# Kernel tuning notes

Hardware: AMD Instinct MI355X
Metric: run time of the kernel (lower is better)

Reference implementation:

```python
import jax, jax.numpy as jnp
import numpy as np


def _safe_norm(d):
    # Euclidean norm over last axis with torch-style subgradient 0 at 0
    sq = jnp.sum(d * d, axis=-1)
    pos = sq > 0
    return jnp.where(pos, jnp.sqrt(jnp.where(pos, sq, 1.0)), 0.0)


def setup_inputs() -> dict:
    key = jax.random.key(0)
    k1, k2 = jax.random.split(key)
    B, n = 8, 256
    src = jax.random.uniform(k1, (B, n, 2), dtype=jnp.float32) * 2.0 - 1.0
    dst = jax.random.uniform(k2, (B, n, 2), dtype=jnp.float32) * 2.0 - 1.0
    return {"src": src, "dst": dst, "s": 256}


def reference(src, dst, s):
    B, n, _ = src.shape
    dt = src.dtype
    # evaluation grid, matching torch.meshgrid(indexing='ij') then stack((ix,iy))
    lin = jnp.linspace(-1.0, 1.0, s, dtype=dt)
    iy, ix = jnp.meshgrid(lin, lin, indexing="ij")
    gs = jnp.stack((ix, iy), axis=2).reshape(1, -1, 2)  # (1, s*s, 2)

    # TPS system: L wv = rhs
    delta = src[:, :, None, :] - src[:, None, :, :]          # (B,n,n,2)
    K = _safe_norm(delta)                                     # (B,n,n)
    P = jnp.concatenate([jnp.ones((B, n, 1), dt), src], 2)    # (B,n,3)
    top = jnp.concatenate([K, P], 2)                          # (B,n,n+3)
    bot = jnp.concatenate([jnp.swapaxes(P, 1, 2),
                           jnp.zeros((B, 3, 3), dt)], 2)      # (B,3,n+3)
    L = jnp.concatenate([top, bot], 1)                        # (B,n+3,n+3)
    rhs = jnp.concatenate([dst, jnp.zeros((B, 3, 2), dt)], 1) # (B,n+3,2)
    wv = jnp.linalg.solve(L, rhs)                             # (B,n+3,2)

    # evaluate warp on the grid
    S = s * s
    dg = gs[:, :, None, :] - src[:, None, :, :]               # (B,S,n,2)
    Kg = _safe_norm(dg)                                       # (B,S,n)
    gsb = jnp.broadcast_to(gs, (B, S, 2))
    Pg = jnp.concatenate([jnp.ones((B, S, 1), dt), gsb], 2)   # (B,S,3)
    Lg = jnp.concatenate([Kg, Pg], 2)                         # (B,S,n+3)
    out = jnp.matmul(Lg, wv)                                  # (B,S,2)
    return out.reshape(B, s, s, 2).transpose(0, 3, 1, 2)
```

## Files before the change

kernel.cpp:

```cpp
#include <hip/hip_runtime.h>
#include <math.h>

#define NCTRL 256
#define NA    259
#define NAUG  261
#define APITCH 264
#define BATCH 8
#define SGRID 256
#define NB    32
#define NPAN  9
#define PPITCH 36
#define PY    4

template<int NBC, int NW>
__device__ __forceinline__ void flat_engine(
    float (&rr)[NBC], const int rows, const int nb, const int width,
    const int tid, const int lane, const int wid,
    float (*panout)[PPITCH], float (*ftmp)[PPITCH], int* permout,
    float (*redrow)[NW][PPITCH], float (*redv)[NW], int (*redi)[NW],
    int* scanw)
{
  bool chosen = false;
  int chosenstep = 0;
  for (int j = 0; j < nb; ++j){
    const int par = j & 1;
    const bool active = (tid < rows) && !chosen;
    float bv = active ? fabsf(rr[0]) : -1.0f;
    int bi = tid;
    #pragma unroll
    for (int off = 32; off; off >>= 1){
      float ov = __shfl_xor(bv, off);
      int   oi = __shfl_xor(bi, off);
      if (ov > bv || (ov == bv && oi < bi)){ bv = ov; bi = oi; }
    }
    if (tid == bi){
      redv[par][wid] = bv; redi[par][wid] = bi;
      #pragma unroll
      for (int q = 0; q < NBC/4; ++q){
        float4 v; v.x=rr[4*q]; v.y=rr[4*q+1]; v.z=rr[4*q+2]; v.w=rr[4*q+3];
        *(float4*)&redrow[par][wid][4*q] = v;
      }
    }
    __syncthreads();
    float gv = redv[par][0]; int gw = 0;
    #pragma unroll
    for (int w = 1; w < NW; ++w){
      if (redv[par][w] > gv ||
          (redv[par][w] == gv && redi[par][w] < redi[par][gw])){
        gv = redv[par][w]; gw = w;
      }
    }
    const int gbi = redi[par][gw];
    float pr[NBC];
    #pragma unroll
    for (int q = 0; q < NBC/4; ++q){
      float4 v = *(const float4*)&redrow[par][gw][4*q];
      pr[4*q]=v.x; pr[4*q+1]=v.y; pr[4*q+2]=v.z; pr[4*q+3]=v.w;
    }
    if (tid < width - j) panout[j][j + tid] = redrow[par][gw][tid];
    if (tid == gbi){ chosen = true; chosenstep = j; }
    if (active && tid != gbi){
      const float rpiv = 1.0f / pr[0];
      const float f = rr[0] * rpiv;
      ftmp[tid][j] = f;
      #pragma unroll
      for (int c = 0; c < NBC-1; ++c)
        rr[c] = fmaf(-f, pr[c+1], rr[c+1]);
    }
  }
  {
    int x = (tid < rows && !chosen) ? 1 : 0;
    int sPS = x;
    #pragma unroll
    for (int off = 1; off < 64; off <<= 1){
      int o = __shfl_up(sPS, off);
      if (lane >= off) sPS += o;
    }
    if (lane == 63) scanw[wid] = sPS;
    __syncthreads();
    int base = 0;
    for (int w = 0; w < wid; ++w) base += scanw[w];
    if (tid < rows){
      const int newloc = chosen ? chosenstep : (nb + base + sPS - x);
      permout[newloc] = tid;
      const int lim = chosen ? chosenstep : nb;
      for (int c = 0; c < lim; ++c) panout[newloc][c] = ftmp[tid][c];
    }
  }
  __syncthreads();
}

__global__ __launch_bounds__(320) void build_panel0(const float* __restrict__ src,
                                                    const float* __restrict__ dst,
                                                    float* __restrict__ A,
                                                    int* __restrict__ permbuf){
  const int b = blockIdx.x;
  float* Ab = A + (size_t)b*NA*APITCH;
  const int tid  = threadIdx.x;
  const int lane = tid & 63;
  const int wid  = tid >> 6;

  __shared__ float pan[NA][PPITCH];
  __shared__ float ftmp[NA][PPITCH];
  __shared__ int   perm[NA];
  __shared__ float redrow[2][5][PPITCH];
  __shared__ float redv[2][5];
  __shared__ int   redi[2][5], scanw[5];
  __shared__ float sx[NCTRL], sy[NCTRL];

  if (tid < NCTRL){
    float2 v = ((const float2*)(src + b*NCTRL*2))[tid];
    sx[tid] = v.x; sy[tid] = v.y;
  }
  __syncthreads();
  {
    const float* db = dst + b*NCTRL*2;
    for (int idx = tid; idx < NA*APITCH; idx += 320){
      int r = idx / APITCH;
      int c = idx - r*APITCH;
      float v = 0.0f;
      if (r < NCTRL){
        if (c < NCTRL){
          float dx = sx[r] - sx[c];
          float dy = sy[r] - sy[c];
          v = __builtin_amdgcn_sqrtf(fmaf(dx, dx, dy*dy));
        } else if (c == NCTRL)   v = 1.0f;
        else if (c == NCTRL+1)   v = sx[r];
        else if (c == NCTRL+2)   v = sy[r];
        else if (c == NA)        v = db[2*r];
        else if (c == NA+1)      v = db[2*r+1];
      } else if (c < NCTRL){
        v = (r == NCTRL) ? 1.0f : ((r == NCTRL+1) ? sx[c] : sy[c]);
      }
      Ab[idx] = v;
      if (c < NB) pan[r][c] = v;
    }
  }
  __syncthreads();

  float rr[NB];
  if (tid < NA){
    #pragma unroll
    for (int q = 0; q < 8; ++q){
      float4 v = *(const float4*)&pan[tid][4*q];
      rr[4*q]=v.x; rr[4*q+1]=v.y; rr[4*q+2]=v.z; rr[4*q+3]=v.w;
    }
  } else {
    #pragma unroll
    for (int c = 0; c < NB; ++c) rr[c] = 0.0f;
  }
  __syncthreads();

  flat_engine<NB,5>(rr, NA, NB, NB, tid, lane, wid,
                    pan, ftmp, perm, redrow, redv, redi, scanw);

  for (int i = tid; i < NA; i += 320) permbuf[b*(NPAN*NA) + i] = perm[i];
  for (int idx = tid; idx < NA*8; idx += 320){
    int i = idx >> 3, q = idx & 7;
    *(float4*)(Ab + (size_t)i*APITCH + 4*q) = *(const float4*)&pan[i][4*q];
  }
}

template<bool LOOK, int NBCN>
__global__ __launch_bounds__(256) void update_kernel(float* __restrict__ A,
                                                     int* __restrict__ permbuf,
                                                     int k0, int pidx, int sb,
                                                     int nbn, int wdn, int wbw){
  const int rows = NA - k0;
  const int ctop = k0 + NB;
  const int tc   = NAUG - ctop;
  const int b    = blockIdx.x / sb;
  const int s    = blockIdx.x - b*sb;
  const int c0   = s*32;
  const int W    = (tc - c0 < 32) ? (tc - c0) : 32;
  float* Ab = A + (size_t)b*NA*APITCH;
  const int tid  = threadIdx.x;
  const int lane = tid & 63;
  const int wid  = tid >> 6;

  __shared__ float pan[NA][PPITCH];
  __shared__ float stage[NA][PPITCH];
  __shared__ float ustg[NB][PPITCH];
  __shared__ int   perm[NA];
  __shared__ float redrow[2][4][PPITCH];
  __shared__ float redv[2][4];
  __shared__ int   redi[2][4], scanw[4];

  for (int i = tid; i < rows; i += 256)
    perm[i] = permbuf[b*(NPAN*NA) + pidx*NA + i];
  for (int idx = tid; idx < rows*8; idx += 256){
    int i = idx >> 3, q = idx & 7;
    *(float4*)&pan[i][4*q] =
      *(const float4*)(Ab + (size_t)(k0+i)*APITCH + k0 + 4*q);
  }
  __syncthreads();

  for (int idx = tid; idx < rows*W; idx += 256){
    int i = idx / W, c = idx - i*W;
    stage[i][c] = Ab[(size_t)(k0+perm[i])*APITCH + ctop + c0 + c];
  }
  __syncthreads();

  if (tid < W){
    float u[NB];
    #pragma unroll
    for (int m = 0; m < NB; ++m) u[m] = stage[m][tid];
    #pragma unroll
    for (int m = 0; m < NB; ++m){
      #pragma unroll
      for (int jj = m+1; jj < NB; ++jj)
        u[jj] = fmaf(-pan[jj][m], u[m], u[jj]);
    }
    #pragma unroll
    for (int m = 0; m < NB; ++m){
      ustg[m][tid] = u[m];
      Ab[(size_t)(k0+m)*APITCH + ctop + c0 + tid] = u[m];
    }
  }
  __syncthreads();

  const int R = rows - NB;
  if (R > 0){
    const int rt = (R + 3) >> 2, ct = (W + 3) >> 2;
    for (int t = tid; t < rt*ct; t += 256){
      int tr = t / ct, tcc = t - tr*ct;
      int i0 = tr*4, cc0 = tcc*4;
      const bool full = (cc0 + 4 <= W);
      int ir[4];
      #pragma unroll
      for (int r = 0; r < 4; ++r){
        int i = i0 + r;
        ir[r] = (i < R) ? i : (R - 1);
      }
      float acc[4][4];
      #pragma unroll
      for (int r = 0; r < 4; ++r){
        if (full){
          float4 v = *(const float4*)&stage[NB + ir[r]][cc0];
          acc[r][0]=v.x; acc[r][1]=v.y; acc[r][2]=v.z; acc[r][3]=v.w;
        } else {
          #pragma unroll
          for (int c = 0; c < 4; ++c)
            acc[r][c] = (cc0 + c < W) ? stage[NB + ir[r]][cc0 + c] : 0.0f;
        }
      }
      #pragma unroll
      for (int mq = 0; mq < NB/4; ++mq){
        float4 lv[4];
        #pragma unroll
        for (int r = 0; r < 4; ++r)
          lv[r] = *(const float4*)&pan[NB + ir[r]][4*mq];
        #pragma unroll
        for (int mi = 0; mi < 4; ++mi){
          float4 uv = *(const float4*)&ustg[4*mq + mi][cc0];
          #pragma unroll
          for (int r = 0; r < 4; ++r){
            float l = (mi==0) ? lv[r].x : (mi==1) ? lv[r].y : (mi==2) ? lv[r].z : lv[r].w;
            acc[r][0] = fmaf(-l, uv.x, acc[r][0]);
            acc[r][1] = fmaf(-l, uv.y, acc[r][1]);
            acc[r][2] = fmaf(-l, uv.z, acc[r][2]);
            acc[r][3] = fmaf(-l, uv.w, acc[r][3]);
          }
        }
      }
      #pragma unroll
      for (int r = 0; r < 4; ++r){
        if (i0 + r < R){
          float* g = Ab + (size_t)(k0 + NB + i0 + r)*APITCH + ctop + c0 + cc0;
          if (full){
            float4 v; v.x=acc[r][0]; v.y=acc[r][1]; v.z=acc[r][2]; v.w=acc[r][3];
            *(float4*)g = v;
            if (LOOK && s == 0) *(float4*)&stage[NB + i0 + r][cc0] = v;
          } else {
            #pragma unroll
            for (int c = 0; c < 4; ++c)
              if (cc0 + c < W){
                g[c] = acc[r][c];
                if (LOOK && s == 0) stage[NB + i0 + r][cc0 + c] = acc[r][c];
              }
          }
        }
      }
    }
  }

  if (LOOK && s == 0){
    __syncthreads();
    const int k0n   = k0 + NB;
    const int rowsN = rows - NB;
    float rr[NBCN];
    if (tid < rowsN){
      #pragma unroll
      for (int q = 0; q < NBCN/4; ++q){
        float4 v = *(const float4*)&stage[NB + tid][4*q];
        rr[4*q]=v.x; rr[4*q+1]=v.y; rr[4*q+2]=v.z; rr[4*q+3]=v.w;
      }
    } else {
      #pragma unroll
      for (int c = 0; c < NBCN; ++c) rr[c] = 0.0f;
    }
    __syncthreads();

    flat_engine<NBCN,4>(rr, rowsN, nbn, wdn, tid, lane, wid,
                        pan, stage, perm, redrow, redv, redi, scanw);

    for (int i = tid; i < rowsN; i += 256)
      permbuf[b*(NPAN*NA) + (pidx+1)*NA + i] = perm[i];
    if (wbw == NB){
      for (int idx = tid; idx < rowsN*8; idx += 256){
        int i = idx >> 3, q = idx & 7;
        *(float4*)(Ab + (size_t)(k0n+i)*APITCH + k0n + 4*q) =
          *(const float4*)&pan[i][4*q];
      }
    } else {
      for (int idx = tid; idx < rowsN*wbw; idx += 256){
        int i = idx / wbw, c = idx - i*wbw;
        Ab[(size_t)(k0n+i)*APITCH + k0n + c] = pan[i][c];
      }
    }
  }
}

__global__ __launch_bounds__(512) void backsub_kernel(const float* __restrict__ A,
                                                      float* __restrict__ wv){
  const int b = blockIdx.x;
  const float* Ab = A + (size_t)b*NA*APITCH;
  const int tid  = threadIdx.x;
  const int lane = tid & 63;
  const int wid  = tid >> 6;

  __shared__ float t2[NA][2];
  __shared__ float xs[NA][2];
  __shared__ float u11[NB][NB+1];

  for (int i = tid; i < NA; i += 512){
    t2[i][0] = Ab[(size_t)i*APITCH + NA];
    t2[i][1] = Ab[(size_t)i*APITCH + NA + 1];
  }
  __syncthreads();

  for (int bp = NPAN-1; bp >= 0; --bp){
    const int k0 = bp*NB;
    const int nb = (NA - k0 < NB) ? (NA - k0) : NB;

    for (int idx = tid; idx < nb*nb; idx += 512){
      int r = idx / nb, c = idx - r*nb;
      u11[r][c] = Ab[(size_t)(k0+r)*APITCH + k0 + c];
    }
    __syncthreads();

    if (wid == 0){
      int j = lane >> 1, ch = lane & 1;
      float tval = (j < nb) ? t2[k0+j][ch] : 0.0f;
      for (int k = nb-1; k >= 0; --k){
        float tk = __shfl(tval, 2*k + ch);
        float xk = tk / u11[k][k];
        if (j <  k) tval = fmaf(-u11[j][k], xk, tval);
        if (j == k) tval = xk;
      }
      if (j < nb) xs[k0+j][ch] = tval;
    }
    __syncthreads();

    if (nb == NB){
      const int q = tid & 7;
      for (int base = 0; base < k0; base += 64){
        const int i = base + (tid >> 3);
        float px = 0.0f, py = 0.0f;
        if (i < k0){
          float4 v = *(const float4*)(Ab + (size_t)i*APITCH + k0 + 4*q);
          px = v.x*xs[k0+4*q+0][0] + v.y*xs[k0+4*q+1][0]
             + v.z*xs[k0+4*q+2][0] + v.w*xs[k0+4*q+3][0];
          py = v.x*xs[k0+4*q+0][1] + v.y*xs[k0+4*q+1][1]
             + v.z*xs[k0+4*q+2][1] + v.w*xs[k0+4*q+3][1];
        }
        px += __shfl_xor(px, 1); px += __shfl_xor(px, 2); px += __shfl_xor(px, 4);
        py += __shfl_xor(py, 1); py += __shfl_xor(py, 2); py += __shfl_xor(py, 4);
        if (q == 0 && i < k0){
          t2[i][0] -= px;
          t2[i][1] -= py;
        }
      }
    } else {
      for (int i = tid; i < k0; i += 512){
        float s0 = 0.0f, s1 = 0.0f;
        #pragma unroll
        for (int m = 0; m < 3; ++m){
          float u = Ab[(size_t)i*APITCH + k0 + m];
          s0 = fmaf(u, xs[k0+m][0], s0);
          s1 = fmaf(u, xs[k0+m][1], s1);
        }
        t2[i][0] -= s0;
        t2[i][1] -= s1;
      }
    }
    __syncthreads();
  }

  for (int i = tid; i < NA; i += 512){
    wv[((size_t)b*NA + i)*2 + 0] = xs[i][0];
    wv[((size_t)b*NA + i)*2 + 1] = xs[i][1];
  }
}

__global__ __launch_bounds__(256) void eval_kernel(const float* __restrict__ src,
                                                   const float* __restrict__ wv,
                                                   float* __restrict__ out){
  const int b  = blockIdx.x >> 6;
  const int yg = blockIdx.x & 63;
  const int xi = threadIdx.x;
  __shared__ float4 cw[NCTRL];
  const float* sb = src + b*NCTRL*2;
  const float* wb = wv + (size_t)b*NA*2;
  {
    float2 sv = ((const float2*)sb)[xi];
    float2 wv2 = ((const float2*)wb)[xi];
    cw[xi] = make_float4(sv.x, sv.y, wv2.x, wv2.y);
  }
  __syncthreads();

  const float step = 2.0f/255.0f;
  const float gx = -1.0f + step*(float)xi;
  const float w0x = wb[512], w1x = wb[514], w2x = wb[516];
  const float w0y = wb[513], w1y = wb[515], w2y = wb[517];

  float gy[PY], ax[PY], ay[PY];
  #pragma unroll
  for (int p = 0; p < PY; ++p){
    gy[p] = -1.0f + step*(float)(yg*PY + p);
    ax[p] = w0x + w1x*gx + w2x*gy[p];
    ay[p] = w0y + w1y*gx + w2y*gy[p];
  }

  #pragma unroll 4
  for (int j = 0; j < NCTRL; ++j){
    float4 c = cw[j];
    float dx = gx - c.x;
    float dx2 = dx*dx;
    #pragma unroll
    for (int p = 0; p < PY; ++p){
      float dy = gy[p] - c.y;
      float r = __builtin_amdgcn_sqrtf(fmaf(dy, dy, dx2));
      ax[p] = fmaf(r, c.z, ax[p]);
      ay[p] = fmaf(r, c.w, ay[p]);
    }
  }

  const int y0 = yg*PY;
  #pragma unroll
  for (int p = 0; p < PY; ++p){
    out[((size_t)(b*2    )*SGRID + y0 + p)*SGRID + xi] = ax[p];
    out[((size_t)(b*2 + 1)*SGRID + y0 + p)*SGRID + xi] = ay[p];
  }
}

extern "C" void kernel_launch(void* const* d_in, const int* in_sizes, int n_in,
                              void* d_out, int out_size, void* d_ws, size_t ws_size,
                              hipStream_t stream) {
  const float* src = (const float*)d_in[0];
  const float* dst = (const float*)d_in[1];
  float* out = (float*)d_out;

  const size_t matElems = (size_t)BATCH*NA*APITCH;
  float* A     = (float*)d_ws;
  float* wv    = A + matElems;
  int*   permb = (int*)(wv + (size_t)BATCH*NA*2);

  build_panel0<<<BATCH, 320, 0, stream>>>(src, dst, A, permb);

  for (int p = 0; p <= 6; ++p){
    const int k0 = p*NB;
    const int tc = NAUG - (k0 + NB);
    const int sb = (tc + 31) >> 5;
    update_kernel<true, NB><<<BATCH*sb, 256, 0, stream>>>(A, permb, k0, p, sb,
                                                          NB, NB, NB);
  }
  update_kernel<true, 8><<<BATCH, 256, 0, stream>>>(A, permb, 7*NB, 7, 1,
                                                    3, 5, 5);

  backsub_kernel<<<BATCH, 512, 0, stream>>>(A, wv);
  eval_kernel<<<BATCH*(SGRID/PY), 256, 0, stream>>>(src, wv, out);
}
```

Measured before the change: 577.8 us.

## Run panel pivoting in a single wavefront and split matrix build into parallel kernel

The pivoted LU panel factorisation used to run across all block threads, paying two __syncthreads and a cross-wave reduction per pivot step. It now runs in a single wavefront where each lane holds several rows in registers, so the per-step argmax is a shuffle reduction followed by a wave barrier. The multiplier buffer is transposed so each step writes coalesced. Building the system matrix moves out of the serial panel kernel into a separate kernel launched over 104 blocks. In exchange, one wave does all the panel arithmetic serially, register pressure rises, and there is an extra launch.

Result: slower. 724.7 us (+25.4%).

```diff
diff --git a/kernel.cpp b/kernel.cpp
--- a/kernel.cpp
+++ b/kernel.cpp
@@ -10,162 +10,201 @@
 #define NB    32
 #define NPAN  9
 #define PPITCH 36
+#define FTP   264
 #define PY    4
 
-template<int NBC, int NW>
-__device__ __forceinline__ void flat_engine(
-    float (&rr)[NBC], const int rows, const int nb, const int width,
-    const int tid, const int lane, const int wid,
-    float (*panout)[PPITCH], float (*ftmp)[PPITCH], int* permout,
-    float (*redrow)[NW][PPITCH], float (*redv)[NW], int (*redi)[NW],
-    int* scanw)
+__global__ __launch_bounds__(256) void build_kernel(const float* __restrict__ src,
+                                                    const float* __restrict__ dst,
+                                                    float* __restrict__ A){
+  const int b = blockIdx.x / 13;
+  const int s = blockIdx.x - b*13;
+  const int r0 = s*20;
+  const int r1 = (r0 + 20 < NA) ? r0 + 20 : NA;
+  const float* sb = src + b*NCTRL*2;
+  const float* db = dst + b*NCTRL*2;
+  float* Ab = A + (size_t)b*NA*APITCH;
+  __shared__ float sx[NCTRL], sy[NCTRL];
+  {
+    int t = threadIdx.x;
+    float2 v = ((const float2*)sb)[t];
+    sx[t] = v.x; sy[t] = v.y;
+  }
+  __syncthreads();
+  const int total = (r1 - r0)*APITCH;
+  for (int idx = threadIdx.x; idx < total; idx += 256){
+    int r = r0 + idx / APITCH;
+    int c = idx % APITCH;
+    float v = 0.0f;
+    if (r < NCTRL){
+      if (c < NCTRL){
+        float dx = sx[r] - sx[c];
+        float dy = sy[r] - sy[c];
+        v = __builtin_amdgcn_sqrtf(fmaf(dx, dx, dy*dy));
+      } else if (c == NCTRL)   v = 1.0f;
+      else if (c == NCTRL+1)   v = sx[r];
+      else if (c == NCTRL+2)   v = sy[r];
+      else if (c == NA)        v = db[2*r];
+      else if (c == NA+1)      v = db[2*r+1];
+    } else if (c < NCTRL){
+      v = (r == NCTRL) ? 1.0f : ((r == NCTRL+1) ? sx[c] : sy[c]);
+    }
+    Ab[(size_t)r*APITCH + c] = v;
+  }
+}
+
+template<int K, int NBC>
+__device__ __forceinline__ void wave_engine(
+    float (&rr)[K][NBC], const int rows, const int nb, const int width,
+    const int lane,
+    float (*panout)[PPITCH], float* prow,
+    float (*ftmp)[FTP], int* stepof)
 {
-  bool chosen = false;
-  int chosenstep = 0;
+  unsigned done = 0;
+  #pragma unroll
+  for (int r = 0; r < K; ++r)
+    if ((r<<6) + lane >= rows) done |= (1u << r);
+
   for (int j = 0; j < nb; ++j){
-    const int par = j & 1;
-    const bool active = (tid < rows) && !chosen;
-    float bv = active ? fabsf(rr[0]) : -1.0f;
-    int bi = tid;
+    float lv = -1.0f; int lq = K << 6;
+    #pragma unroll
+    for (int r = 0; r < K; ++r){
+      float a = ((done >> r) & 1u) ? -1.0f : fabsf(rr[r][0]);
+      int q = (r << 6) | lane;
+      if (a > lv || (a == lv && q < lq)){ lv = a; lq = q; }
+    }
     #pragma unroll
     for (int off = 32; off; off >>= 1){
-      float ov = __shfl_xor(bv, off);
-      int   oi = __shfl_xor(bi, off);
-      if (ov > bv || (ov == bv && oi < bi)){ bv = ov; bi = oi; }
-    }
-    if (tid == bi){
-      redv[par][wid] = bv; redi[par][wid] = bi;
-      #pragma unroll
-      for (int q = 0; q < NBC/4; ++q){
-        float4 v; v.x=rr[4*q]; v.y=rr[4*q+1]; v.z=rr[4*q+2]; v.w=rr[4*q+3];
-        *(float4*)&redrow[par][wid][4*q] = v;
-      }
-    }
-    __syncthreads();
-    float gv = redv[par][0]; int gw = 0;
-    #pragma unroll
-    for (int w = 1; w < NW; ++w){
-      if (redv[par][w] > gv ||
-          (redv[par][w] == gv && redi[par][w] < redi[par][gw])){
-        gv = redv[par][w]; gw = w;
-      }
-    }
-    const int gbi = redi[par][gw];
+      float ov = __shfl_xor(lv, off);
+      int   oq = __shfl_xor(lq, off);
+      if (ov > lv || (ov == lv && oq < lq)){ lv = ov; lq = oq; }
+    }
+    const int src_lane = lq & 63;
+    const int src_r    = lq >> 6;
+    if (lane == src_lane){
+      #pragma unroll
+      for (int r = 0; r < K; ++r){
+        if (r == src_r){
+          #pragma unroll
+          for (int q = 0; q < NBC/4; ++q){
+            float4 v; v.x=rr[r][4*q]; v.y=rr[r][4*q+1];
+            v.z=rr[r][4*q+2]; v.w=rr[r][4*q+3];
+            *(float4*)&prow[4*q] = v;
+          }
+        }
+      }
+      stepof[lq] = j;
+      done |= (1u << src_r);
+    }
+    __builtin_amdgcn_wave_barrier();
     float pr[NBC];
     #pragma unroll
     for (int q = 0; q < NBC/4; ++q){
-      float4 v = *(const float4*)&redrow[par][gw][4*q];
+      float4 v = *(const float4*)&prow[4*q];
       pr[4*q]=v.x; pr[4*q+1]=v.y; pr[4*q+2]=v.z; pr[4*q+3]=v.w;
     }
-    if (tid < width - j) panout[j][j + tid] = redrow[par][gw][tid];
-    if (tid == gbi){ chosen = true; chosenstep = j; }
-    if (active && tid != gbi){
-      const float rpiv = 1.0f / pr[0];
-      const float f = rr[0] * rpiv;
-      ftmp[tid][j] = f;
+    if (lane < width - j) panout[j][j + lane] = prow[lane];
+    const float rpiv = 1.0f / pr[0];
+    #pragma unroll
+    for (int r = 0; r < K; ++r){
+      const float f = rr[r][0] * rpiv;
+      if (!((done >> r) & 1u)) ftmp[j][(r<<6) + lane] = f;
       #pragma unroll
       for (int c = 0; c < NBC-1; ++c)
-        rr[c] = fmaf(-f, pr[c+1], rr[c+1]);
-    }
-  }
-  {
-    int x = (tid < rows && !chosen) ? 1 : 0;
-    int sPS = x;
-    #pragma unroll
-    for (int off = 1; off < 64; off <<= 1){
-      int o = __shfl_up(sPS, off);
-      if (lane >= off) sPS += o;
-    }
-    if (lane == 63) scanw[wid] = sPS;
-    __syncthreads();
-    int base = 0;
-    for (int w = 0; w < wid; ++w) base += scanw[w];
-    if (tid < rows){
-      const int newloc = chosen ? chosenstep : (nb + base + sPS - x);
-      permout[newloc] = tid;
-      const int lim = chosen ? chosenstep : nb;
-      for (int c = 0; c < lim; ++c) panout[newloc][c] = ftmp[tid][c];
-    }
-  }
-  __syncthreads();
-}
-
-__global__ __launch_bounds__(320) void build_panel0(const float* __restrict__ src,
-                                                    const float* __restrict__ dst,
-                                                    float* __restrict__ A,
-                                                    int* __restrict__ permbuf){
+        rr[r][c] = fmaf(-f, pr[c+1], rr[r][c+1]);
+      rr[r][NBC-1] = 0.0f;
+    }
+    __builtin_amdgcn_wave_barrier();
+  }
+}
+
+template<int NW, int NT>
+__device__ __forceinline__ void panel_epilogue(
+    const int rows, const int nb, const int tid, const int lane, const int wid,
+    float (*panout)[PPITCH], float (*ftmp)[FTP],
+    const int* stepof, int* permout, int* scanw)
+{
+  const int st = (tid < rows) ? stepof[tid] : -1;
+  const bool chosen = (tid < rows) && (st >= 0);
+  int x = (tid < rows && !chosen) ? 1 : 0;
+  int s = x;
+  #pragma unroll
+  for (int off = 1; off < 64; off <<= 1){
+    int o = __shfl_up(s, off);
+    if (lane >= off) s += o;
+  }
+  if (lane == 63) scanw[wid] = s;
+  __syncthreads();
+  int base = 0;
+  for (int w = 0; w < wid; ++w) base += scanw[w];
+  if (tid < rows){
+    const int newloc = chosen ? st : (nb + base + s - x);
+    permout[newloc] = tid;
+    const int lim = chosen ? st : nb;
+    for (int c = 0; c < lim; ++c) panout[newloc][c] = ftmp[c][tid];
+  }
+  __syncthreads();
+}
+
+__global__ __launch_bounds__(320, 1) void panel0_kernel(const float* __restrict__ src,
+                                                        float* __restrict__ A,
+                                                        int* __restrict__ permbuf){
   const int b = blockIdx.x;
   float* Ab = A + (size_t)b*NA*APITCH;
-  const int tid  = threadIdx.x;
-  const int lane = tid & 63;
-  const int wid  = tid >> 6;
+  const int tid = threadIdx.x, lane = tid & 63, wid = tid >> 6;
 
   __shared__ float pan[NA][PPITCH];
-  __shared__ float ftmp[NA][PPITCH];
+  __shared__ float ftmp[NB][FTP];
+  __shared__ float prow[NB];
+  __shared__ int   stepof[NA];
   __shared__ int   perm[NA];
-  __shared__ float redrow[2][5][PPITCH];
-  __shared__ float redv[2][5];
-  __shared__ int   redi[2][5], scanw[5];
-  __shared__ float sx[NCTRL], sy[NCTRL];
-
-  if (tid < NCTRL){
-    float2 v = ((const float2*)(src + b*NCTRL*2))[tid];
-    sx[tid] = v.x; sy[tid] = v.y;
-  }
-  __syncthreads();
-  {
-    const float* db = dst + b*NCTRL*2;
-    for (int idx = tid; idx < NA*APITCH; idx += 320){
-      int r = idx / APITCH;
-      int c = idx - r*APITCH;
-      float v = 0.0f;
-      if (r < NCTRL){
-        if (c < NCTRL){
-          float dx = sx[r] - sx[c];
-          float dy = sy[r] - sy[c];
-          v = __builtin_amdgcn_sqrtf(fmaf(dx, dx, dy*dy));
-        } else if (c == NCTRL)   v = 1.0f;
-        else if (c == NCTRL+1)   v = sx[r];
-        else if (c == NCTRL+2)   v = sy[r];
-        else if (c == NA)        v = db[2*r];
-        else if (c == NA+1)      v = db[2*r+1];
-      } else if (c < NCTRL){
-        v = (r == NCTRL) ? 1.0f : ((r == NCTRL+1) ? sx[c] : sy[c]);
-      }
-      Ab[idx] = v;
-      if (c < NB) pan[r][c] = v;
-    }
-  }
-  __syncthreads();
-
-  float rr[NB];
-  if (tid < NA){
-    #pragma unroll
-    for (int q = 0; q < 8; ++q){
-      float4 v = *(const float4*)&pan[tid][4*q];
-      rr[4*q]=v.x; rr[4*q+1]=v.y; rr[4*q+2]=v.z; rr[4*q+3]=v.w;
-    }
-  } else {
-    #pragma unroll
-    for (int c = 0; c < NB; ++c) rr[c] = 0.0f;
-  }
-  __syncthreads();
-
-  flat_engine<NB,5>(rr, NA, NB, NB, tid, lane, wid,
-                    pan, ftmp, perm, redrow, redv, redi, scanw);
-
-  for (int i = tid; i < NA; i += 320) permbuf[b*(NPAN*NA) + i] = perm[i];
+  __shared__ int   scanw[5];
+  __shared__ float2 sxy[NCTRL];
+
+  if (tid < NCTRL) sxy[tid] = ((const float2*)(src + b*NCTRL*2))[tid];
+  for (int i = tid; i < NA; i += 320) stepof[i] = -1;
+  __syncthreads();
+
+  if (wid == 0){
+    float rr[5][NB];
+    #pragma unroll
+    for (int r = 0; r < 5; ++r){
+      const int row = (r<<6) + lane;
+      if (row < NCTRL){
+        const float rx = sxy[row].x, ry = sxy[row].y;
+        #pragma unroll
+        for (int c = 0; c < NB; ++c){
+          float dx = rx - sxy[c].x, dy = ry - sxy[c].y;
+          rr[r][c] = __builtin_amdgcn_sqrtf(fmaf(dx, dx, dy*dy));
+        }
+      } else if (row < NA){
+        #pragma unroll
+        for (int c = 0; c < NB; ++c)
+          rr[r][c] = (row == NCTRL) ? 1.0f
+                   : ((row == NCTRL+1) ? sxy[c].x : sxy[c].y);
+      } else {
+        #pragma unroll
+        for (int c = 0; c < NB; ++c) rr[r][c] = 0.0f;
+      }
+    }
+    wave_engine<5, NB>(rr, NA, NB, NB, lane, pan, prow, ftmp, stepof);
+  }
+  __syncthreads();
+
+  panel_epilogue<5, 320>(NA, NB, tid, lane, wid, pan, ftmp, stepof, perm, scanw);
+
+  for (int i = tid; i < NA; i += 320)
+    permbuf[b*(NPAN*NA) + i] = perm[i];
   for (int idx = tid; idx < NA*8; idx += 320){
     int i = idx >> 3, q = idx & 7;
     *(float4*)(Ab + (size_t)i*APITCH + 4*q) = *(const float4*)&pan[i][4*q];
   }
 }
 
-template<bool LOOK, int NBCN>
-__global__ __launch_bounds__(256) void update_kernel(float* __restrict__ A,
-                                                     int* __restrict__ permbuf,
-                                                     int k0, int pidx, int sb,
-                                                     int nbn, int wdn, int wbw){
+template<bool LOOK, int KK, int NBCN>
+__global__ __launch_bounds__(256, 1) void update_kernel(float* __restrict__ A,
+                                                        int* __restrict__ permbuf,
+                                                        int k0, int pidx, int sb,
+                                                        int nbn, int wdn, int wbw){
   const int rows = NA - k0;
   const int ctop = k0 + NB;
   const int tc   = NAUG - ctop;
@@ -181,10 +220,11 @@
   __shared__ float pan[NA][PPITCH];
   __shared__ float stage[NA][PPITCH];
   __shared__ float ustg[NB][PPITCH];
+  __shared__ float ftmp[NB][FTP];
+  __shared__ float prow[NB];
   __shared__ int   perm[NA];
-  __shared__ float redrow[2][4][PPITCH];
-  __shared__ float redv[2][4];
-  __shared__ int   redi[2][4], scanw[4];
+  __shared__ int   stepof[NA];
+  __shared__ int   scanw[4];
 
   for (int i = tid; i < rows; i += 256)
     perm[i] = permbuf[b*(NPAN*NA) + pidx*NA + i];
@@ -288,24 +328,32 @@
     __syncthreads();
     const int k0n   = k0 + NB;
     const int rowsN = rows - NB;
-    float rr[NBCN];
-    if (tid < rowsN){
-      #pragma unroll
-      for (int q = 0; q < NBCN/4; ++q){
-        float4 v = *(const float4*)&stage[NB + tid][4*q];
-        rr[4*q]=v.x; rr[4*q+1]=v.y; rr[4*q+2]=v.z; rr[4*q+3]=v.w;
-      }
-    } else {
-      #pragma unroll
-      for (int c = 0; c < NBCN; ++c) rr[c] = 0.0f;
-    }
+    for (int i = tid; i < rowsN; i += 256) stepof[i] = -1;
     __syncthreads();
 
-    flat_engine<NBCN,4>(rr, rowsN, nbn, wdn, tid, lane, wid,
-                        pan, stage, perm, redrow, redv, redi, scanw);
-
-    for (int i = tid; i < rowsN; i += 256)
-      permbuf[b*(NPAN*NA) + (pidx+1)*NA + i] = perm[i];
+    if (wid == 0){
+      float rr[KK][NBCN];
+      #pragma unroll
+      for (int r = 0; r < KK; ++r){
+        const int row = (r<<6) + lane;
+        if (row < rowsN){
+          #pragma unroll
+          for (int q = 0; q < NBCN/4; ++q){
+            float4 v = *(const float4*)&stage[NB + row][4*q];
+            rr[r][4*q]=v.x; rr[r][4*q+1]=v.y; rr[r][4*q+2]=v.z; rr[r][4*q+3]=v.w;
+          }
+        } else {
+          #pragma unroll
+          for (int c = 0; c < NBCN; ++c) rr[r][c] = 0.0f;
+        }
+      }
+      wave_engine<KK, NBCN>(rr, rowsN, nbn, wdn, lane, pan, prow, ftmp, stepof);
+    }
+    __syncthreads();
+
+    panel_epilogue<4, 256>(rowsN, nbn, tid, lane, wid, pan, ftmp, stepof,
+                           permbuf + b*(NPAN*NA) + (pidx+1)*NA, scanw);
+
     if (wbw == NB){
       for (int idx = tid; idx < rowsN*8; idx += 256){
         int i = idx >> 3, q = idx & 7;
@@ -466,17 +514,25 @@
   float* wv    = A + matElems;
   int*   permb = (int*)(wv + (size_t)BATCH*NA*2);
 
-  build_panel0<<<BATCH, 320, 0, stream>>>(src, dst, A, permb);
-
-  for (int p = 0; p <= 6; ++p){
-    const int k0 = p*NB;
-    const int tc = NAUG - (k0 + NB);
-    const int sb = (tc + 31) >> 5;
-    update_kernel<true, NB><<<BATCH*sb, 256, 0, stream>>>(A, permb, k0, p, sb,
-                                                          NB, NB, NB);
-  }
-  update_kernel<true, 8><<<BATCH, 256, 0, stream>>>(A, permb, 7*NB, 7, 1,
-                                                    3, 5, 5);
+  build_kernel<<<BATCH*13, 256, 0, stream>>>(src, dst, A);
+  panel0_kernel<<<BATCH, 320, 0, stream>>>(src, A, permb);
+
+  {
+    const int kk[7] = {4, 4, 3, 3, 2, 2, 1};
+    for (int p = 0; p <= 6; ++p){
+      const int k0 = p*NB;
+      const int tc = NAUG - (k0 + NB);
+      const int sb = (tc + 31) >> 5;
+      const int grid = BATCH*sb;
+      switch (kk[p]){
+        case 4: update_kernel<true,4,NB><<<grid,256,0,stream>>>(A,permb,k0,p,sb,NB,NB,NB); break;
+        case 3: update_kernel<true,3,NB><<<grid,256,0,stream>>>(A,permb,k0,p,sb,NB,NB,NB); break;
+        case 2: update_kernel<true,2,NB><<<grid,256,0,stream>>>(A,permb,k0,p,sb,NB,NB,NB); break;
+        default:update_kernel<true,1,NB><<<grid,256,0,stream>>>(A,permb,k0,p,sb,NB,NB,NB); break;
+      }
+    }
+  }
+  update_kernel<true,1,8><<<BATCH, 256, 0, stream>>>(A, permb, 7*NB, 7, 1, 3, 5, 5);
 
   backsub_kernel<<<BATCH, 512, 0, stream>>>(A, wv);
   eval_kernel<<<BATCH*(SGRID/PY), 256, 0, stream>>>(src, wv, out);
```
